# Performance work log

Measured on AMD Instinct MI355X. Metric: run time of the kernel, lower is better.

Reference implementation:

```python
import jax, jax.numpy as jnp
import numpy as np

EPS = 1e-5
POW = 0.5

def _eig_fun(X, fn):
    # symmetric matrix function via eigendecomposition: V f(diag) V^T
    w, V = jnp.linalg.eigh(X)
    return jnp.einsum('...ij,...j,...kj->...ik', V, fn(w), V)

def sym_pow(X, p):
    return _eig_fun(X, lambda w: jnp.power(w, p))

def sym_log(X):
    return _eig_fun(X, jnp.log)

def sym_exp(X):
    return _eig_fun(X, jnp.exp)

def exp_at(T, G):
    # Riemannian exp of tangent T at base point G (affine-invariant metric)
    Gh = sym_pow(G, 0.5)
    Gnh = sym_pow(G, -0.5)
    return Gh @ sym_exp(Gnh @ T @ Gnh) @ Gh

def bary_geom(X, n_iter=1):
    # Karcher/geodesic mean of batch of SPD matrices X: (B, n, n)
    # init at arithmetic mean, n_iter Karcher flow steps
    G = jnp.mean(X, axis=0)
    for _ in range(n_iter):
        Gh = sym_pow(G, 0.5)
        Gnh = sym_pow(G, -0.5)
        T = jnp.mean(sym_log(Gnh @ X @ Gnh), axis=0)
        G = Gh @ sym_exp(T) @ Gh
    return G

def setup_inputs() -> dict:
    key = jax.random.key(0)
    N, h, n = 256, 16, 64
    k1, k2, k3 = jax.random.split(key, 3)
    A = jax.random.normal(k1, (N, h, n, n), dtype=jnp.float32)
    # well-conditioned SPD inputs with distinct eigenvalues
    X = A @ jnp.swapaxes(A, -1, -2) / n + 0.5 * jnp.eye(n, dtype=jnp.float32)
    Bw = jax.random.normal(k2, (n, n), dtype=jnp.float32) * 0.1
    weight = sym_exp(0.5 * (Bw + Bw.T))  # SPD parameter near identity
    Bm = jax.random.normal(k3, (n, n), dtype=jnp.float32) * 0.1
    M = sym_exp(0.5 * (Bm + Bm.T))       # SPD deformation parameter
    shift = jnp.ones((1,), dtype=jnp.float32)
    return {"X": X, "weight": weight, "M": M, "shift": shift}

def reference(X, weight, M, shift):
    N, h, n, _ = X.shape
    Xb = X.reshape(N * h, n, n)
    Xp = sym_pow(Xb, POW)                  # PowerEig(X, po)
    Mnh = sym_pow(M, -0.5)
    Mh = sym_pow(M, 0.5)
    Xc = Mnh @ Xp @ Mnh                    # CongrG(., M, 'neg')
    Wp = sym_pow(weight, POW)              # PowerEig(weight, po)
    Wc = Mnh @ Wp @ Mnh                    # CongrG1(weight, M, 'neg')

    mean = bary_geom(Xc)                   # BaryGeom (training path)
    mnh = sym_pow(mean, -0.5)
    # pal1(mean, LogG(Xc, mean)) = PT of Riemannian log to identity
    T = sym_log(mnh @ Xc @ mnh)            # (N*h, n, n) tangent at I
    # cal_var: mean squared Riemannian distance to the mean
    var = jnp.mean(jnp.sum(T * T, axis=(-2, -1)))
    T = T * (shift[0] / jnp.sqrt(var + EPS))  # scale1
    Wh = sym_pow(weight, 0.5)
    S = Wh @ T @ Wh                        # pal2(weight, LogG1(.))
    Y = exp_at(S, Wc)                      # ExpG(., weight_deformed)
    Y = Mh @ Y @ Mh                        # CongrG(., M, 'pos')
    Y = sym_pow(Y, 1.0 / POW)              # PowerEig(., 1/po)
    return Y.reshape(N, h, n, n)
```

## Files before the change

### kernel.cpp

```cpp
#include <hip/hip_runtime.h>
#include <math.h>

#define PITCH 72
#define NP 68
#define SW_BATCH 12
#define SW_SMALL 10
#define NPART 32
#define EPS2_ROT 1e-12f

#define KATTR __attribute__((amdgpu_flat_work_group_size(256, 256), amdgpu_waves_per_eu(1, 2)))

#define OFF_ACCG 0
#define OFF_ACCT (NPART*4096)
#define OFF_BASE (2*NPART*4096)
#define SL_MNH  (OFF_BASE + 0*4096)
#define SL_MH   (OFF_BASE + 1*4096)
#define SL_WH   (OFF_BASE + 2*4096)
#define SL_P    (OFF_BASE + 3*4096)
#define SL_Q    (OFF_BASE + 4*4096)
#define SL_GH   (OFF_BASE + 5*4096)
#define SL_GNH  (OFF_BASE + 6*4096)
#define SL_MNH2 (OFF_BASE + 7*4096)
#define SL_WCH  (OFF_BASE + 8*4096)
#define OFF_VAR (OFF_BASE + 9*4096)
#define SL_SC   (OFF_BASE + 9*4096 + 1)

struct __align__(16) F4 { float v[4]; };

struct __align__(16) Smem {
  float S0[64*PITCH];
  float S1[64*PITCH];
  float w2[64];
  float wc[64];
  float red[256];
};

__device__ __forceinline__ void g2s(float* dst, const float* __restrict__ src) {
  int t = threadIdx.x;
#pragma unroll
  for (int i = 0; i < 4; ++i) {
    int e4 = t + (i << 8);
    F4 vv = *(const F4*)&src[e4 * 4];
    *(F4*)&dst[(e4 >> 4) * PITCH + (e4 & 15) * 4] = vv;
  }
  __syncthreads();
}
__device__ __forceinline__ void s2g(float* __restrict__ dst, const float* src) {
  int t = threadIdx.x;
#pragma unroll
  for (int i = 0; i < 4; ++i) {
    int e4 = t + (i << 8);
    F4 vv = *(const F4*)&src[(e4 >> 4) * PITCH + (e4 & 15) * 4];
    *(F4*)&dst[e4 * 4] = vv;
  }
  __syncthreads();
}

template<int MODE>
__device__ void mmX(Smem& sm) {
  int t = threadIdx.x;
  int R0 = t >> 4;
  int J = (t & 15) * 4;
  float acc[4][4] = {};
  for (int kb = 0; kb < 64; kb += 4) {
    F4 a4[4], b4[4];
#pragma unroll
    for (int i = 0; i < 4; ++i) {
      const float* L = (MODE == 0) ? sm.S1 : sm.S0;
      a4[i] = *(const F4*)&L[(R0 + 16 * i) * PITCH + kb];
    }
#pragma unroll
    for (int kk = 0; kk < 4; ++kk) {
      const float* Rp = (MODE == 0) ? sm.S0 : sm.S1;
      b4[kk] = *(const F4*)&Rp[(kb + kk) * PITCH + J];
    }
#pragma unroll
    for (int i = 0; i < 4; ++i)
#pragma unroll
      for (int kk = 0; kk < 4; ++kk)
#pragma unroll
        for (int m = 0; m < 4; ++m)
          acc[i][m] = fmaf(a4[i].v[kk], b4[kk].v[m], acc[i][m]);
  }
  __syncthreads();
#pragma unroll
  for (int i = 0; i < 4; ++i) {
    F4 o;
#pragma unroll
    for (int m = 0; m < 4; ++m) o.v[m] = acc[i][m];
    *(F4*)&sm.S0[(R0 + 16 * i) * PITCH + J] = o;
  }
  __syncthreads();
}

__device__ void reconT(Smem& sm) {
  __syncthreads();
  int t = threadIdx.x;
  int R0 = t >> 4;
  int J = (t & 15) * 4;
  float acc[4][4] = {};
  for (int k = 0; k < 64; ++k) {
    float w = sm.wc[k];
    float a[4];
#pragma unroll
    for (int i = 0; i < 4; ++i) a[i] = w * sm.S0[k * PITCH + R0 + 16 * i];
    F4 b = *(const F4*)&sm.S0[k * PITCH + J];
#pragma unroll
    for (int i = 0; i < 4; ++i)
#pragma unroll
      for (int m = 0; m < 4; ++m) acc[i][m] = fmaf(a[i], b.v[m], acc[i][m]);
  }
#pragma unroll
  for (int i = 0; i < 4; ++i) {
    F4 o;
#pragma unroll
    for (int m = 0; m < 4; ++m) o.v[m] = acc[i][m];
    *(F4*)&sm.S1[(R0 + 16 * i) * PITCH + J] = o;
  }
  __syncthreads();
}

__device__ float frob2(Smem& sm) {
  int t = threadIdx.x;
  float s = 0.f;
#pragma unroll
  for (int i = 0; i < 4; ++i) {
    int e4 = t + (i << 8);
    F4 vv = *(const F4*)&sm.S0[(e4 >> 4) * PITCH + (e4 & 15) * 4];
#pragma unroll
    for (int m = 0; m < 4; ++m) s = fmaf(vv.v[m], vv.v[m], s);
  }
  sm.red[t] = s;
  __syncthreads();
  for (int o = 128; o; o >>= 1) { if (t < o) sm.red[t] += sm.red[t + o]; __syncthreads(); }
  float f = sm.red[0];
  __syncthreads();
  return f;
}

__device__ __forceinline__ void hestenes_reg(float (&own)[64], float& w2out, int sweeps) {
  const int lane = threadIdx.x & 63;
  float nrm = 0.f;
#pragma unroll
  for (int i = 0; i < 64; ++i) nrm = fmaf(own[i], own[i], nrm);

  for (int s = 0; s < sweeps; ++s) {
    bool any = false;
    for (int m = 1; m < 64; ++m) {
      const int paddr = ((lane ^ m) << 2);
      float pv[64];
#pragma unroll
      for (int i = 0; i < 64; ++i)
        asm volatile("ds_bpermute_b32 %0, %1, %2"
                     : "=v"(pv[i]) : "v"(paddr), "v"(own[i]));
      asm volatile("s_waitcnt lgkmcnt(0)" ::: "memory");
      __builtin_amdgcn_sched_barrier(0);
      float d0 = 0.f, d1 = 0.f, d2 = 0.f, d3 = 0.f;
#pragma unroll
      for (int i = 0; i < 64; i += 4) {
        d0 = fmaf(own[i + 0], pv[i + 0], d0);
        d1 = fmaf(own[i + 1], pv[i + 1], d1);
        d2 = fmaf(own[i + 2], pv[i + 2], d2);
        d3 = fmaf(own[i + 3], pv[i + 3], d3);
      }
      float d = (d0 + d1) + (d2 + d3);
      float pn = __shfl_xor(nrm, m);
      if (d * d > EPS2_ROT * (nrm * pn)) {
        any = true;
        bool lo = lane < (lane ^ m);
        float dpp = lo ? nrm : pn;
        float dqq = lo ? pn : nrm;
        float tau = (dqq - dpp) * (0.5f * __builtin_amdgcn_rcpf(d));
        float tt = __builtin_amdgcn_rcpf(fabsf(tau) +
                                         __builtin_amdgcn_sqrtf(fmaf(tau, tau, 1.f)));
        if (tau < 0.f) tt = -tt;
        float c = __builtin_amdgcn_rsqf(fmaf(tt, tt, 1.f));
        float s_ = tt * c;
        float sg = lo ? -s_ : s_;
#pragma unroll
        for (int i = 0; i < 64; ++i) own[i] = fmaf(sg, pv[i], c * own[i]);
        float td = tt * d;
        nrm += lo ? -td : td;
      }
    }
    if (!__any((int)any)) break;
  }
  float w = 0.f;
#pragma unroll
  for (int i = 0; i < 64; ++i) w = fmaf(own[i], own[i], w);
  w2out = w;
}

__device__ void hestenes_small(Smem& sm, int sweeps) {
  const int t = threadIdx.x;
  if (t < 64) {
    float own[64];
#pragma unroll
    for (int i = 0; i < 64; ++i) own[i] = sm.S0[t * PITCH + i];
    float w2;
    hestenes_reg(own, w2, sweeps);
#pragma unroll
    for (int i = 0; i < 64; ++i) sm.S0[t * PITCH + i] = own[i];
    sm.w2[t] = w2;
  }
  __syncthreads();
}

struct __align__(16) SmemK {
  float A[64*NP];
  float Bop[64*NP];
  float wc[64];
  float red[256];
};
struct __align__(16) SmemK4 {
  float A[64*NP];
  float P[64*NP];
  float Q[64*NP];
  float wc[64];
  float red[256];
};

__device__ __forceinline__ void g2s68(float* dst, const float* __restrict__ src) {
  int t = threadIdx.x;
#pragma unroll
  for (int i = 0; i < 4; ++i) {
    int e4 = t + (i << 8);
    F4 vv = *(const F4*)&src[e4 * 4];
    *(F4*)&dst[(e4 >> 4) * NP + (e4 & 15) * 4] = vv;
  }
  __syncthreads();
}
__device__ __forceinline__ void g2s68s(float* dst, const float* __restrict__ src, float sc) {
  int t = threadIdx.x;
#pragma unroll
  for (int i = 0; i < 4; ++i) {
    int e4 = t + (i << 8);
    F4 vv = *(const F4*)&src[e4 * 4];
#pragma unroll
    for (int m = 0; m < 4; ++m) vv.v[m] *= sc;
    *(F4*)&dst[(e4 >> 4) * NP + (e4 & 15) * 4] = vv;
  }
  __syncthreads();
}

template<int MODE>
__device__ void mm68(float* A, const float* Bo) {
  int t = threadIdx.x;
  int R0 = t >> 4;
  if (MODE == 2) {
    int J0 = t & 15;
    float acc[4][4] = {};
    for (int kb = 0; kb < 64; kb += 4) {
      F4 a4[4];
#pragma unroll
      for (int i = 0; i < 4; ++i) a4[i] = *(const F4*)&A[(R0 + 16 * i) * NP + kb];
#pragma unroll
      for (int kk = 0; kk < 4; ++kk) {
        float b[4];
#pragma unroll
        for (int m = 0; m < 4; ++m) b[m] = Bo[(J0 + 16 * m) * NP + kb + kk];
#pragma unroll
        for (int i = 0; i < 4; ++i)
#pragma unroll
          for (int m = 0; m < 4; ++m) acc[i][m] = fmaf(a4[i].v[kk], b[m], acc[i][m]);
      }
    }
    __syncthreads();
#pragma unroll
    for (int i = 0; i < 4; ++i)
#pragma unroll
      for (int m = 0; m < 4; ++m)
        A[(R0 + 16 * i) * NP + J0 + 16 * m] = acc[i][m];
    __syncthreads();
  } else {
    int J = (t & 15) * 4;
    float acc[4][4] = {};
    for (int kb = 0; kb < 64; kb += 4) {
      F4 a4[4], b4[4];
#pragma unroll
      for (int i = 0; i < 4; ++i) {
        const float* L = (MODE == 0) ? Bo : A;
        a4[i] = *(const F4*)&L[(R0 + 16 * i) * NP + kb];
      }
#pragma unroll
      for (int kk = 0; kk < 4; ++kk) {
        const float* Rp = (MODE == 0) ? A : Bo;
        b4[kk] = *(const F4*)&Rp[(kb + kk) * NP + J];
      }
#pragma unroll
      for (int i = 0; i < 4; ++i)
#pragma unroll
        for (int kk = 0; kk < 4; ++kk)
#pragma unroll
          for (int m = 0; m < 4; ++m)
            acc[i][m] = fmaf(a4[i].v[kk], b4[kk].v[m], acc[i][m]);
    }
    __syncthreads();
#pragma unroll
    for (int i = 0; i < 4; ++i) {
      F4 o;
#pragma unroll
      for (int m = 0; m < 4; ++m) o.v[m] = acc[i][m];
      *(F4*)&A[(R0 + 16 * i) * NP + J] = o;
    }
    __syncthreads();
  }
}

__device__ float frob68(const float* A, float* red) {
  int t = threadIdx.x;
  float s = 0.f;
#pragma unroll
  for (int i = 0; i < 4; ++i) {
    int e4 = t + (i << 8);
    F4 vv = *(const F4*)&A[(e4 >> 4) * NP + (e4 & 15) * 4];
#pragma unroll
    for (int m = 0; m < 4; ++m) s = fmaf(vv.v[m], vv.v[m], s);
  }
  red[t] = s;
  __syncthreads();
  for (int o = 128; o; o >>= 1) { if (t < o) red[t] += red[t + o]; __syncthreads(); }
  float f = red[0];
  __syncthreads();
  return f;
}

__device__ void msq_store(const float* Z, float* __restrict__ gout) {
  int t = threadIdx.x;
  int R0 = t >> 4;
  int J = (t & 15) * 4;
  float acc[4][4] = {};
  for (int kb = 0; kb < 64; kb += 4) {
    F4 a4[4], b4[4];
#pragma unroll
    for (int i = 0; i < 4; ++i) a4[i] = *(const F4*)&Z[(R0 + 16 * i) * NP + kb];
#pragma unroll
    for (int kk = 0; kk < 4; ++kk) b4[kk] = *(const F4*)&Z[(kb + kk) * NP + J];
#pragma unroll
    for (int i = 0; i < 4; ++i)
#pragma unroll
      for (int kk = 0; kk < 4; ++kk)
#pragma unroll
        for (int m = 0; m < 4; ++m)
          acc[i][m] = fmaf(a4[i].v[kk], b4[kk].v[m], acc[i][m]);
  }
#pragma unroll
  for (int i = 0; i < 4; ++i) {
    F4 o;
#pragma unroll
    for (int m = 0; m < 4; ++m) o.v[m] = acc[i][m];
    *(F4*)&gout[(R0 + 16 * i) * 64 + J] = o;
  }
}


__global__ __launch_bounds__(256) void kzero(float* ws) {
  int i = blockIdx.x * 256 + threadIdx.x;
  if (i < OFF_BASE) ws[i] = 0.f;
  if (i == 0) ws[OFF_VAR] = 0.f;
}

__global__ KATTR void kprep(const float* __restrict__ weight,
                            const float* __restrict__ M,
                            float* ws) {
  __shared__ Smem sm;
  int t = threadIdx.x;
  g2s(sm.S0, M);
  hestenes_small(sm, SW_SMALL);
  if (t < 64) sm.wc[t] = powf(fmaxf(sm.w2[t], 1e-12f), -1.25f);
  reconT(sm); s2g(ws + SL_MNH, sm.S1);
  if (t < 64) sm.wc[t] = powf(fmaxf(sm.w2[t], 1e-12f), -0.75f);
  reconT(sm); s2g(ws + SL_MH, sm.S1);

  g2s(sm.S0, weight);
  hestenes_small(sm, SW_SMALL);
  if (t < 64) sm.wc[t] = powf(fmaxf(sm.w2[t], 1e-12f), -0.75f);
  reconT(sm); s2g(ws + SL_WH, sm.S1);

  g2s(sm.S0, ws + SL_MNH);
  mmX<1>(sm);
  g2s(sm.S1, ws + SL_MNH);
  mmX<1>(sm);
  hestenes_small(sm, SW_SMALL);
  if (t < 64) sm.wc[t] = powf(fmaxf(sm.w2[t], 1e-12f), -0.75f);
  reconT(sm); s2g(ws + SL_WCH, sm.S1);
  if (t < 64) sm.wc[t] = powf(fmaxf(sm.w2[t], 1e-12f), -1.25f);
  reconT(sm);
  g2s(sm.S0, ws + SL_WH);
  mmX<0>(sm);
  s2g(ws + SL_P, sm.S0);
  g2s(sm.S0, ws + SL_WCH);
  g2s(sm.S1, ws + SL_MH);
  mmX<0>(sm);
  s2g(ws + SL_Q, sm.S0);
}

__global__ KATTR void k1(const float* __restrict__ X,
                         float* __restrict__ out, float* ws) {
  __shared__ SmemK sm;
  int t = threadIdx.x;
  int w = t >> 6, lane = t & 63;
  size_t b = blockIdx.x;
  g2s68(sm.Bop, ws + SL_MNH);

  float own[64]; float w2;
  {
    const float* Xm = X + (b * 4 + w) * 4096 + (size_t)lane * 64;
#pragma unroll
    for (int j = 0; j < 16; ++j) {
      F4 r = *(const F4*)&Xm[4 * j];
      own[4 * j + 0] = r.v[0]; own[4 * j + 1] = r.v[1];
      own[4 * j + 2] = r.v[2]; own[4 * j + 3] = r.v[3];
    }
  }
  hestenes_reg(own, w2, SW_BATCH);
  __syncthreads();

  int R0 = t >> 4, J = (t & 15) * 4;
  for (int m = 0; m < 4; ++m) {
    if (w == m) {
#pragma unroll
      for (int j = 0; j < 16; ++j) {
        F4 o = {{own[4 * j], own[4 * j + 1], own[4 * j + 2], own[4 * j + 3]}};
        *(F4*)&sm.A[lane * NP + 4 * j] = o;
      }
      sm.wc[lane] = powf(fmaxf(w2, 1e-12f), -0.75f);
    }
    __syncthreads();
    mm68<1>(sm.A, sm.Bop);
    float acc[4][4] = {};
    for (int k = 0; k < 64; ++k) {
      float wck = sm.wc[k];
      float a[4];
#pragma unroll
      for (int i = 0; i < 4; ++i) a[i] = wck * sm.A[k * NP + R0 + 16 * i];
      F4 bb = *(const F4*)&sm.A[k * NP + J];
#pragma unroll
      for (int i = 0; i < 4; ++i)
#pragma unroll
        for (int mc = 0; mc < 4; ++mc) acc[i][mc] = fmaf(a[i], bb.v[mc], acc[i][mc]);
    }
    float* Xc = out + (b * 4 + m) * 4096;
    float* accp = ws + OFF_ACCG + (size_t)((b * 4 + m) & (NPART - 1)) * 4096;
#pragma unroll
    for (int i = 0; i < 4; ++i) {
      F4 o;
#pragma unroll
      for (int mc = 0; mc < 4; ++mc) o.v[mc] = acc[i][mc];
      int base = (R0 + 16 * i) * 64 + J;
      *(F4*)&Xc[base] = o;
#pragma unroll
      for (int mc = 0; mc < 4; ++mc) atomicAdd(accp + base + mc, o.v[mc]);
    }
    __syncthreads();
  }
}

__global__ KATTR void ksmall2(float* ws, float invB) {
  __shared__ Smem sm;
  int t = threadIdx.x;
#pragma unroll
  for (int i = 0; i < 4; ++i) {
    int e4 = t + (i << 8);
    F4 sum = {{0.f, 0.f, 0.f, 0.f}};
    for (int p = 0; p < NPART; ++p) {
      F4 vv = *(const F4*)&ws[OFF_ACCG + p * 4096 + e4 * 4];
#pragma unroll
      for (int m = 0; m < 4; ++m) sum.v[m] += vv.v[m];
    }
#pragma unroll
    for (int m = 0; m < 4; ++m) sum.v[m] *= invB;
    *(F4*)&sm.S0[(e4 >> 4) * PITCH + (e4 & 15) * 4] = sum;
  }
  __syncthreads();
  hestenes_small(sm, SW_SMALL);
  if (t < 64) sm.wc[t] = powf(fmaxf(sm.w2[t], 1e-12f), -0.75f);
  reconT(sm); s2g(ws + SL_GH, sm.S1);
  if (t < 64) sm.wc[t] = powf(fmaxf(sm.w2[t], 1e-12f), -1.25f);
  reconT(sm); s2g(ws + SL_GNH, sm.S1);
}

__global__ KATTR void k2(const float* __restrict__ XcBuf, float* ws) {
  __shared__ SmemK sm;
  int t = threadIdx.x;
  int w = t >> 6, lane = t & 63;
  size_t b = blockIdx.x;
  g2s68(sm.Bop, ws + SL_GNH);

  float own[64]; float w2;
  for (int m = 0; m < 4; ++m) {
    g2s68(sm.A, XcBuf + (b * 4 + m) * 4096);
    mm68<1>(sm.A, sm.Bop);
    mm68<0>(sm.A, sm.Bop);
    if (w == m) {
#pragma unroll
      for (int i = 0; i < 64; ++i) own[i] = sm.A[i * NP + lane];
    }
    __syncthreads();
  }
  hestenes_reg(own, w2, SW_BATCH);
  __syncthreads();

  int R0 = t >> 4, J = (t & 15) * 4;
  for (int m = 0; m < 4; ++m) {
    if (w == m) {
#pragma unroll
      for (int j = 0; j < 16; ++j) {
        F4 o = {{own[4 * j], own[4 * j + 1], own[4 * j + 2], own[4 * j + 3]}};
        *(F4*)&sm.A[lane * NP + 4 * j] = o;
      }
      float s2 = fmaxf(w2, 1e-12f);
      sm.wc[lane] = 0.5f * logf(s2) / s2;
    }
    __syncthreads();
    float acc[4][4] = {};
    for (int k = 0; k < 64; ++k) {
      float wck = sm.wc[k];
      float a[4];
#pragma unroll
      for (int i = 0; i < 4; ++i) a[i] = wck * sm.A[k * NP + R0 + 16 * i];
      F4 bb = *(const F4*)&sm.A[k * NP + J];
#pragma unroll
      for (int i = 0; i < 4; ++i)
#pragma unroll
        for (int mc = 0; mc < 4; ++mc) acc[i][mc] = fmaf(a[i], bb.v[mc], acc[i][mc]);
    }
    float* accp = ws + OFF_ACCT + (size_t)((b * 4 + m) & (NPART - 1)) * 4096;
#pragma unroll
    for (int i = 0; i < 4; ++i) {
      int base = (R0 + 16 * i) * 64 + J;
#pragma unroll
      for (int mc = 0; mc < 4; ++mc) atomicAdd(accp + base + mc, acc[i][mc]);
    }
    __syncthreads();
  }
}

__global__ KATTR void ksmall3(float* ws, float invB) {
  __shared__ Smem sm;
  int t = threadIdx.x;
#pragma unroll
  for (int i = 0; i < 4; ++i) {
    int e4 = t + (i << 8);
    F4 sum = {{0.f, 0.f, 0.f, 0.f}};
    for (int p = 0; p < NPART; ++p) {
      F4 vv = *(const F4*)&ws[OFF_ACCT + p * 4096 + e4 * 4];
#pragma unroll
      for (int m = 0; m < 4; ++m) sum.v[m] += vv.v[m];
    }
#pragma unroll
    for (int m = 0; m < 4; ++m) sum.v[m] *= invB;
    *(F4*)&sm.S0[(e4 >> 4) * PITCH + (e4 & 15) * 4] = sum;
  }
  __syncthreads();
  float mu = sqrtf(frob2(sm)) + 1e-3f;
  if (t < 64) sm.S0[t * PITCH + t] += mu;
  __syncthreads();
  hestenes_small(sm, SW_SMALL);
  if (t < 64) {
    float s2 = fmaxf(sm.w2[t], 1e-12f);
    sm.wc[t] = expf(sqrtf(s2) - mu) / s2;
  }
  reconT(sm);
  g2s(sm.S0, ws + SL_GH);
  mmX<1>(sm);
  g2s(sm.S1, ws + SL_GH);
  mmX<1>(sm);
  hestenes_small(sm, SW_SMALL);
  if (t < 64) sm.wc[t] = powf(fmaxf(sm.w2[t], 1e-12f), -1.25f);
  reconT(sm); s2g(ws + SL_MNH2, sm.S1);
}

__global__ KATTR void k3(float* __restrict__ buf, float* ws) {
  __shared__ SmemK sm;
  int t = threadIdx.x;
  int w = t >> 6, lane = t & 63;
  size_t b = blockIdx.x;
  g2s68(sm.Bop, ws + SL_MNH2);

  float own[64]; float w2;
  for (int m = 0; m < 4; ++m) {
    g2s68(sm.A, buf + (b * 4 + m) * 4096);
    mm68<1>(sm.A, sm.Bop);
    mm68<0>(sm.A, sm.Bop);
    if (w == m) {
#pragma unroll
      for (int i = 0; i < 64; ++i) own[i] = sm.A[i * NP + lane];
    }
    __syncthreads();
  }
  hestenes_reg(own, w2, SW_BATCH);
  __syncthreads();

  int R0 = t >> 4, J = (t & 15) * 4;
  for (int m = 0; m < 4; ++m) {
    if (w == m) {
#pragma unroll
      for (int j = 0; j < 16; ++j) {
        F4 o = {{own[4 * j], own[4 * j + 1], own[4 * j + 2], own[4 * j + 3]}};
        *(F4*)&sm.A[lane * NP + 4 * j] = o;
      }
      float s2 = fmaxf(w2, 1e-12f);
      sm.wc[lane] = 0.5f * logf(s2) / s2;
    }
    __syncthreads();
    float acc[4][4] = {};
    for (int k = 0; k < 64; ++k) {
      float wck = sm.wc[k];
      float a[4];
#pragma unroll
      for (int i = 0; i < 4; ++i) a[i] = wck * sm.A[k * NP + R0 + 16 * i];
      F4 bb = *(const F4*)&sm.A[k * NP + J];
#pragma unroll
      for (int i = 0; i < 4; ++i)
#pragma unroll
        for (int mc = 0; mc < 4; ++mc) acc[i][mc] = fmaf(a[i], bb.v[mc], acc[i][mc]);
    }
    float* Tg = buf + (b * 4 + m) * 4096;
    float ssq = 0.f;
#pragma unroll
    for (int i = 0; i < 4; ++i) {
      F4 o;
#pragma unroll
      for (int mc = 0; mc < 4; ++mc) o.v[mc] = acc[i][mc];
      int base = (R0 + 16 * i) * 64 + J;
      *(F4*)&Tg[base] = o;
#pragma unroll
      for (int mc = 0; mc < 4; ++mc) ssq = fmaf(o.v[mc], o.v[mc], ssq);
    }
    sm.red[t] = ssq;
    __syncthreads();
    for (int o = 128; o; o >>= 1) { if (t < o) sm.red[t] += sm.red[t + o]; __syncthreads(); }
    if (t == 0) atomicAdd(ws + OFF_VAR, sm.red[0]);
    __syncthreads();
  }
}

__global__ void kscale(float* ws, const float* __restrict__ shift, float invB) {
  if (threadIdx.x == 0 && blockIdx.x == 0) {
    float var = ws[OFF_VAR] * invB;
    ws[SL_SC] = shift[0] / sqrtf(var + 1e-5f);
  }
}

__global__ KATTR void k4(float* __restrict__ buf, float* ws) {
  __shared__ SmemK4 sm;
  int t = threadIdx.x;
  int w = t >> 6, lane = t & 63;
  size_t b = blockIdx.x;
  float sc = ws[SL_SC];
  g2s68(sm.P, ws + SL_P);
  g2s68(sm.Q, ws + SL_Q);

  float own[64]; float w2; float muw = 0.f;
  for (int m = 0; m < 4; ++m) {
    g2s68s(sm.A, buf + (b * 4 + m) * 4096, sc);
    mm68<0>(sm.A, sm.P);
    mm68<2>(sm.A, sm.P);
    float f = frob68(sm.A, sm.red);
    if (w == m) {
      muw = sqrtf(f) + 1e-3f;
#pragma unroll
      for (int i = 0; i < 64; ++i) {
        float v = sm.A[i * NP + lane];
        own[i] = v + ((i == lane) ? muw : 0.f);
      }
    }
    __syncthreads();
  }
  hestenes_reg(own, w2, SW_BATCH);
  __syncthreads();

  int R0 = t >> 4, J = (t & 15) * 4;
  for (int m = 0; m < 4; ++m) {
    if (w == m) {
#pragma unroll
      for (int j = 0; j < 16; ++j) {
        F4 o = {{own[4 * j], own[4 * j + 1], own[4 * j + 2], own[4 * j + 3]}};
        *(F4*)&sm.A[lane * NP + 4 * j] = o;
      }
      float s2 = fmaxf(w2, 1e-12f);
      sm.wc[lane] = expf(sqrtf(s2) - muw) / s2;
    }
    __syncthreads();
    mm68<2>(sm.A, sm.Q);
    float acc[4][4] = {};
    for (int k = 0; k < 64; ++k) {
      float wck = sm.wc[k];
      float a[4];
#pragma unroll
      for (int i = 0; i < 4; ++i) a[i] = wck * sm.A[k * NP + R0 + 16 * i];
      F4 bb = *(const F4*)&sm.A[k * NP + J];
#pragma unroll
      for (int i = 0; i < 4; ++i)
#pragma unroll
        for (int mc = 0; mc < 4; ++mc) acc[i][mc] = fmaf(a[i], bb.v[mc], acc[i][mc]);
    }
#pragma unroll
    for (int i = 0; i < 4; ++i) {
      F4 o;
#pragma unroll
      for (int mc = 0; mc < 4; ++mc) o.v[mc] = acc[i][mc];
      *(F4*)&sm.P[(R0 + 16 * i) * NP + J] = o;
    }
    __syncthreads();
    msq_store(sm.P, buf + (b * 4 + m) * 4096);
    __syncthreads();
  }
}

extern "C" void kernel_launch(void* const* d_in, const int* in_sizes, int n_in,
                              void* d_out, int out_size, void* d_ws, size_t ws_size,
                              hipStream_t stream) {
  const float* X      = (const float*)d_in[0];
  const float* weight = (const float*)d_in[1];
  const float* M      = (const float*)d_in[2];
  const float* shift  = (const float*)d_in[3];
  float* out = (float*)d_out;
  float* ws  = (float*)d_ws;
  int B = in_sizes[0] / 4096;
  float invB = 1.f / (float)B;
  int G = B / 4;

  hipLaunchKernelGGL(kzero,   dim3(OFF_BASE / 256), dim3(256), 0, stream, ws);
  hipLaunchKernelGGL(kprep,   dim3(1), dim3(256), 0, stream, weight, M, ws);
  hipLaunchKernelGGL(k1,      dim3(G), dim3(256), 0, stream, X, out, ws);
  hipLaunchKernelGGL(ksmall2, dim3(1), dim3(256), 0, stream, ws, invB);
  hipLaunchKernelGGL(k2,      dim3(G), dim3(256), 0, stream, out, ws);
  hipLaunchKernelGGL(ksmall3, dim3(1), dim3(256), 0, stream, ws, invB);
  hipLaunchKernelGGL(k3,      dim3(G), dim3(256), 0, stream, out, ws);
  hipLaunchKernelGGL(kscale,  dim3(1), dim3(64), 0, stream, ws, shift, invB);
  hipLaunchKernelGGL(k4,      dim3(G), dim3(256), 0, stream, out, ws);
}
```

Before: 9.408 ms.

## Split Jacobi eigensolver into standalone 64-thread kernel, separate GEMM stages

Moves the one-sided Hestenes Jacobi sweep out of the fused 256-thread kernels into a dedicated 64-thread-per-matrix kernel launched once per stage. Each GEMM/congruence stage becomes its own high-occupancy kernel that reads the rotated columns back and recomputes the squared eigenvalues from row norms. k3 now uses a precomputed combined matrix R and a pre-kernel instead of re-running congruence inside the eigensolver kernel. It also swaps inline-asm bpermute for __shfl_xor. The goal is to decouple the register-heavy eigensolver from the LDS-heavy matmuls so each can reach better occupancy, at the cost of extra launches and extra global round-trips of the batch buffer.

```diff
diff --git a/kernel.cpp b/kernel.cpp
--- a/kernel.cpp
+++ b/kernel.cpp
@@ -8,14 +8,13 @@
 #define NPART 32
 #define EPS2_ROT 1e-12f
 
-#define KATTR __attribute__((amdgpu_flat_work_group_size(256, 256), amdgpu_waves_per_eu(1, 2)))
-
 #define OFF_ACCG 0
 #define OFF_ACCT (NPART*4096)
 #define OFF_BASE (2*NPART*4096)
 #define SL_MNH  (OFF_BASE + 0*4096)
 #define SL_MH   (OFF_BASE + 1*4096)
 #define SL_WH   (OFF_BASE + 2*4096)
+#define SL_MU   SL_WH
 #define SL_P    (OFF_BASE + 3*4096)
 #define SL_Q    (OFF_BASE + 4*4096)
 #define SL_GH   (OFF_BASE + 5*4096)
@@ -24,119 +23,9 @@
 #define SL_WCH  (OFF_BASE + 8*4096)
 #define OFF_VAR (OFF_BASE + 9*4096)
 #define SL_SC   (OFF_BASE + 9*4096 + 1)
+#define SL_R    (OFF_BASE + 10*4096)
 
 struct __align__(16) F4 { float v[4]; };
-
-struct __align__(16) Smem {
-  float S0[64*PITCH];
-  float S1[64*PITCH];
-  float w2[64];
-  float wc[64];
-  float red[256];
-};
-
-__device__ __forceinline__ void g2s(float* dst, const float* __restrict__ src) {
-  int t = threadIdx.x;
-#pragma unroll
-  for (int i = 0; i < 4; ++i) {
-    int e4 = t + (i << 8);
-    F4 vv = *(const F4*)&src[e4 * 4];
-    *(F4*)&dst[(e4 >> 4) * PITCH + (e4 & 15) * 4] = vv;
-  }
-  __syncthreads();
-}
-__device__ __forceinline__ void s2g(float* __restrict__ dst, const float* src) {
-  int t = threadIdx.x;
-#pragma unroll
-  for (int i = 0; i < 4; ++i) {
-    int e4 = t + (i << 8);
-    F4 vv = *(const F4*)&src[(e4 >> 4) * PITCH + (e4 & 15) * 4];
-    *(F4*)&dst[e4 * 4] = vv;
-  }
-  __syncthreads();
-}
-
-template<int MODE>
-__device__ void mmX(Smem& sm) {
-  int t = threadIdx.x;
-  int R0 = t >> 4;
-  int J = (t & 15) * 4;
-  float acc[4][4] = {};
-  for (int kb = 0; kb < 64; kb += 4) {
-    F4 a4[4], b4[4];
-#pragma unroll
-    for (int i = 0; i < 4; ++i) {
-      const float* L = (MODE == 0) ? sm.S1 : sm.S0;
-      a4[i] = *(const F4*)&L[(R0 + 16 * i) * PITCH + kb];
-    }
-#pragma unroll
-    for (int kk = 0; kk < 4; ++kk) {
-      const float* Rp = (MODE == 0) ? sm.S0 : sm.S1;
-      b4[kk] = *(const F4*)&Rp[(kb + kk) * PITCH + J];
-    }
-#pragma unroll
-    for (int i = 0; i < 4; ++i)
-#pragma unroll
-      for (int kk = 0; kk < 4; ++kk)
-#pragma unroll
-        for (int m = 0; m < 4; ++m)
-          acc[i][m] = fmaf(a4[i].v[kk], b4[kk].v[m], acc[i][m]);
-  }
-  __syncthreads();
-#pragma unroll
-  for (int i = 0; i < 4; ++i) {
-    F4 o;
-#pragma unroll
-    for (int m = 0; m < 4; ++m) o.v[m] = acc[i][m];
-    *(F4*)&sm.S0[(R0 + 16 * i) * PITCH + J] = o;
-  }
-  __syncthreads();
-}
-
-__device__ void reconT(Smem& sm) {
-  __syncthreads();
-  int t = threadIdx.x;
-  int R0 = t >> 4;
-  int J = (t & 15) * 4;
-  float acc[4][4] = {};
-  for (int k = 0; k < 64; ++k) {
-    float w = sm.wc[k];
-    float a[4];
-#pragma unroll
-    for (int i = 0; i < 4; ++i) a[i] = w * sm.S0[k * PITCH + R0 + 16 * i];
-    F4 b = *(const F4*)&sm.S0[k * PITCH + J];
-#pragma unroll
-    for (int i = 0; i < 4; ++i)
-#pragma unroll
-      for (int m = 0; m < 4; ++m) acc[i][m] = fmaf(a[i], b.v[m], acc[i][m]);
-  }
-#pragma unroll
-  for (int i = 0; i < 4; ++i) {
-    F4 o;
-#pragma unroll
-    for (int m = 0; m < 4; ++m) o.v[m] = acc[i][m];
-    *(F4*)&sm.S1[(R0 + 16 * i) * PITCH + J] = o;
-  }
-  __syncthreads();
-}
-
-__device__ float frob2(Smem& sm) {
-  int t = threadIdx.x;
-  float s = 0.f;
-#pragma unroll
-  for (int i = 0; i < 4; ++i) {
-    int e4 = t + (i << 8);
-    F4 vv = *(const F4*)&sm.S0[(e4 >> 4) * PITCH + (e4 & 15) * 4];
-#pragma unroll
-    for (int m = 0; m < 4; ++m) s = fmaf(vv.v[m], vv.v[m], s);
-  }
-  sm.red[t] = s;
-  __syncthreads();
-  for (int o = 128; o; o >>= 1) { if (t < o) sm.red[t] += sm.red[t + o]; __syncthreads(); }
-  float f = sm.red[0];
-  __syncthreads();
-  return f;
-}
 
 __device__ __forceinline__ void hestenes_reg(float (&own)[64], float& w2out, int sweeps) {
   const int lane = threadIdx.x & 63;
@@ -147,14 +36,9 @@
   for (int s = 0; s < sweeps; ++s) {
     bool any = false;
     for (int m = 1; m < 64; ++m) {
-      const int paddr = ((lane ^ m) << 2);
       float pv[64];
 #pragma unroll
-      for (int i = 0; i < 64; ++i)
-        asm volatile("ds_bpermute_b32 %0, %1, %2"
-                     : "=v"(pv[i]) : "v"(paddr), "v"(own[i]));
-      asm volatile("s_waitcnt lgkmcnt(0)" ::: "memory");
-      __builtin_amdgcn_sched_barrier(0);
+      for (int i = 0; i < 64; ++i) pv[i] = __shfl_xor(own[i], m);
       float d0 = 0.f, d1 = 0.f, d2 = 0.f, d3 = 0.f;
 #pragma unroll
       for (int i = 0; i < 64; i += 4) {
@@ -191,6 +75,139 @@
   w2out = w;
 }
 
+__global__ __launch_bounds__(64, 1) void keig(float* __restrict__ buf,
+                                              const float* __restrict__ src) {
+  const int l = threadIdx.x;
+  const size_t b = blockIdx.x;
+  const float* Sm = src + b * 4096 + (size_t)l * 64;
+  float own[64];
+#pragma unroll
+  for (int j = 0; j < 16; ++j) {
+    F4 r = *(const F4*)&Sm[4 * j];
+    own[4 * j + 0] = r.v[0]; own[4 * j + 1] = r.v[1];
+    own[4 * j + 2] = r.v[2]; own[4 * j + 3] = r.v[3];
+  }
+  float w2;
+  hestenes_reg(own, w2, SW_BATCH);
+  float* Dm = buf + b * 4096 + (size_t)l * 64;
+#pragma unroll
+  for (int j = 0; j < 16; ++j) {
+    F4 o = {{own[4 * j], own[4 * j + 1], own[4 * j + 2], own[4 * j + 3]}};
+    *(F4*)&Dm[4 * j] = o;
+  }
+}
+
+struct __align__(16) Smem {
+  float S0[64*PITCH];
+  float S1[64*PITCH];
+  float w2[64];
+  float wc[64];
+  float red[256];
+};
+
+__device__ __forceinline__ void g2s(float* dst, const float* __restrict__ src) {
+  int t = threadIdx.x;
+#pragma unroll
+  for (int i = 0; i < 4; ++i) {
+    int e4 = t + (i << 8);
+    F4 vv = *(const F4*)&src[e4 * 4];
+    *(F4*)&dst[(e4 >> 4) * PITCH + (e4 & 15) * 4] = vv;
+  }
+  __syncthreads();
+}
+__device__ __forceinline__ void s2g(float* __restrict__ dst, const float* src) {
+  int t = threadIdx.x;
+#pragma unroll
+  for (int i = 0; i < 4; ++i) {
+    int e4 = t + (i << 8);
+    F4 vv = *(const F4*)&src[(e4 >> 4) * PITCH + (e4 & 15) * 4];
+    *(F4*)&dst[e4 * 4] = vv;
+  }
+  __syncthreads();
+}
+
+template<int MODE>
+__device__ void mmX(Smem& sm) {
+  int t = threadIdx.x;
+  int R0 = t >> 4;
+  int J = (t & 15) * 4;
+  float acc[4][4] = {};
+  for (int kb = 0; kb < 64; kb += 4) {
+    F4 a4[4], b4[4];
+#pragma unroll
+    for (int i = 0; i < 4; ++i) {
+      const float* L = (MODE == 0) ? sm.S1 : sm.S0;
+      a4[i] = *(const F4*)&L[(R0 + 16 * i) * PITCH + kb];
+    }
+#pragma unroll
+    for (int kk = 0; kk < 4; ++kk) {
+      const float* Rp = (MODE == 0) ? sm.S0 : sm.S1;
+      b4[kk] = *(const F4*)&Rp[(kb + kk) * PITCH + J];
+    }
+#pragma unroll
+    for (int i = 0; i < 4; ++i)
+#pragma unroll
+      for (int kk = 0; kk < 4; ++kk)
+#pragma unroll
+        for (int m = 0; m < 4; ++m)
+          acc[i][m] = fmaf(a4[i].v[kk], b4[kk].v[m], acc[i][m]);
+  }
+  __syncthreads();
+#pragma unroll
+  for (int i = 0; i < 4; ++i) {
+    F4 o;
+#pragma unroll
+    for (int m = 0; m < 4; ++m) o.v[m] = acc[i][m];
+    *(F4*)&sm.S0[(R0 + 16 * i) * PITCH + J] = o;
+  }
+  __syncthreads();
+}
+
+__device__ void reconT(Smem& sm) {
+  __syncthreads();
+  int t = threadIdx.x;
+  int R0 = t >> 4;
+  int J = (t & 15) * 4;
+  float acc[4][4] = {};
+  for (int k = 0; k < 64; ++k) {
+    float w = sm.wc[k];
+    float a[4];
+#pragma unroll
+    for (int i = 0; i < 4; ++i) a[i] = w * sm.S0[k * PITCH + R0 + 16 * i];
+    F4 b = *(const F4*)&sm.S0[k * PITCH + J];
+#pragma unroll
+    for (int i = 0; i < 4; ++i)
+#pragma unroll
+      for (int m = 0; m < 4; ++m) acc[i][m] = fmaf(a[i], b.v[m], acc[i][m]);
+  }
+#pragma unroll
+  for (int i = 0; i < 4; ++i) {
+    F4 o;
+#pragma unroll
+    for (int m = 0; m < 4; ++m) o.v[m] = acc[i][m];
+    *(F4*)&sm.S1[(R0 + 16 * i) * PITCH + J] = o;
+  }
+  __syncthreads();
+}
+
+__device__ float frob2(Smem& sm) {
+  int t = threadIdx.x;
+  float s = 0.f;
+#pragma unroll
+  for (int i = 0; i < 4; ++i) {
+    int e4 = t + (i << 8);
+    F4 vv = *(const F4*)&sm.S0[(e4 >> 4) * PITCH + (e4 & 15) * 4];
+#pragma unroll
+    for (int m = 0; m < 4; ++m) s = fmaf(vv.v[m], vv.v[m], s);
+  }
+  sm.red[t] = s;
+  __syncthreads();
+  for (int o = 128; o; o >>= 1) { if (t < o) sm.red[t] += sm.red[t + o]; __syncthreads(); }
+  float f = sm.red[0];
+  __syncthreads();
+  return f;
+}
+
 __device__ void hestenes_small(Smem& sm, int sweeps) {
   const int t = threadIdx.x;
   if (t < 64) {
@@ -212,13 +229,6 @@
   float wc[64];
   float red[256];
 };
-struct __align__(16) SmemK4 {
-  float A[64*NP];
-  float P[64*NP];
-  float Q[64*NP];
-  float wc[64];
-  float red[256];
-};
 
 __device__ __forceinline__ void g2s68(float* dst, const float* __restrict__ src) {
   int t = threadIdx.x;
@@ -241,6 +251,23 @@
     *(F4*)&dst[(e4 >> 4) * NP + (e4 & 15) * 4] = vv;
   }
   __syncthreads();
+}
+__device__ __forceinline__ void s2g68(float* __restrict__ dst, const float* src) {
+  int t = threadIdx.x;
+#pragma unroll
+  for (int i = 0; i < 4; ++i) {
+    int e4 = t + (i << 8);
+    F4 vv = *(const F4*)&src[(e4 >> 4) * NP + (e4 & 15) * 4];
+    *(F4*)&dst[e4 * 4] = vv;
+  }
+  __syncthreads();
+}
+
+__device__ __forceinline__ float rown2(const float* A, int t) {
+  float s = 0.f;
+#pragma unroll
+  for (int j = 0; j < 64; ++j) { float v = A[t * NP + j]; s = fmaf(v, v, s); }
+  return fmaxf(s, 1e-12f);
 }
 
 template<int MODE>
@@ -360,9 +387,9 @@
   if (i == 0) ws[OFF_VAR] = 0.f;
 }
 
-__global__ KATTR void kprep(const float* __restrict__ weight,
-                            const float* __restrict__ M,
-                            float* ws) {
+__global__ __launch_bounds__(256, 1) void kprep(const float* __restrict__ weight,
+                                                const float* __restrict__ M,
+                                                float* ws) {
   __shared__ Smem sm;
   int t = threadIdx.x;
   g2s(sm.S0, M);
@@ -395,37 +422,16 @@
   s2g(ws + SL_Q, sm.S0);
 }
 
-__global__ KATTR void k1(const float* __restrict__ X,
-                         float* __restrict__ out, float* ws) {
+__global__ __launch_bounds__(256, 4) void k1b(float* __restrict__ buf, float* ws) {
   __shared__ SmemK sm;
   int t = threadIdx.x;
-  int w = t >> 6, lane = t & 63;
   size_t b = blockIdx.x;
   g2s68(sm.Bop, ws + SL_MNH);
-
-  float own[64]; float w2;
-  {
-    const float* Xm = X + (b * 4 + w) * 4096 + (size_t)lane * 64;
-#pragma unroll
-    for (int j = 0; j < 16; ++j) {
-      F4 r = *(const F4*)&Xm[4 * j];
-      own[4 * j + 0] = r.v[0]; own[4 * j + 1] = r.v[1];
-      own[4 * j + 2] = r.v[2]; own[4 * j + 3] = r.v[3];
-    }
-  }
-  hestenes_reg(own, w2, SW_BATCH);
-  __syncthreads();
-
   int R0 = t >> 4, J = (t & 15) * 4;
   for (int m = 0; m < 4; ++m) {
-    if (w == m) {
-#pragma unroll
-      for (int j = 0; j < 16; ++j) {
-        F4 o = {{own[4 * j], own[4 * j + 1], own[4 * j + 2], own[4 * j + 3]}};
-        *(F4*)&sm.A[lane * NP + 4 * j] = o;
-      }
-      sm.wc[lane] = powf(fmaxf(w2, 1e-12f), -0.75f);
-    }
+    size_t bm = b * 4 + m;
+    g2s68(sm.A, buf + bm * 4096);
+    if (t < 64) sm.wc[t] = powf(rown2(sm.A, t), -0.75f);
     __syncthreads();
     mm68<1>(sm.A, sm.Bop);
     float acc[4][4] = {};
@@ -440,8 +446,8 @@
 #pragma unroll
         for (int mc = 0; mc < 4; ++mc) acc[i][mc] = fmaf(a[i], bb.v[mc], acc[i][mc]);
     }
-    float* Xc = out + (b * 4 + m) * 4096;
-    float* accp = ws + OFF_ACCG + (size_t)((b * 4 + m) & (NPART - 1)) * 4096;
+    float* Xc = buf + bm * 4096;
+    float* accp = ws + OFF_ACCG + (size_t)(bm & (NPART - 1)) * 4096;
 #pragma unroll
     for (int i = 0; i < 4; ++i) {
       F4 o;
@@ -456,7 +462,7 @@
   }
 }
 
-__global__ KATTR void ksmall2(float* ws, float invB) {
+__global__ __launch_bounds__(256, 1) void ksmall2(float* ws, float invB) {
   __shared__ Smem sm;
   int t = threadIdx.x;
 #pragma unroll
@@ -480,37 +486,30 @@
   reconT(sm); s2g(ws + SL_GNH, sm.S1);
 }
 
-__global__ KATTR void k2(const float* __restrict__ XcBuf, float* ws) {
+__global__ __launch_bounds__(256, 4) void kcongr(float* __restrict__ buf, float* ws) {
   __shared__ SmemK sm;
-  int t = threadIdx.x;
-  int w = t >> 6, lane = t & 63;
   size_t b = blockIdx.x;
   g2s68(sm.Bop, ws + SL_GNH);
-
-  float own[64]; float w2;
   for (int m = 0; m < 4; ++m) {
-    g2s68(sm.A, XcBuf + (b * 4 + m) * 4096);
+    size_t bm = b * 4 + m;
+    g2s68(sm.A, buf + bm * 4096);
     mm68<1>(sm.A, sm.Bop);
     mm68<0>(sm.A, sm.Bop);
-    if (w == m) {
-#pragma unroll
-      for (int i = 0; i < 64; ++i) own[i] = sm.A[i * NP + lane];
-    }
-    __syncthreads();
-  }
-  hestenes_reg(own, w2, SW_BATCH);
-  __syncthreads();
-
+    s2g68(buf + bm * 4096, sm.A);
+  }
+}
+
+__global__ __launch_bounds__(256, 4) void k2b(const float* __restrict__ buf, float* ws) {
+  __shared__ SmemK sm;
+  int t = threadIdx.x;
+  size_t b = blockIdx.x;
   int R0 = t >> 4, J = (t & 15) * 4;
   for (int m = 0; m < 4; ++m) {
-    if (w == m) {
-#pragma unroll
-      for (int j = 0; j < 16; ++j) {
-        F4 o = {{own[4 * j], own[4 * j + 1], own[4 * j + 2], own[4 * j + 3]}};
-        *(F4*)&sm.A[lane * NP + 4 * j] = o;
-      }
-      float s2 = fmaxf(w2, 1e-12f);
-      sm.wc[lane] = 0.5f * logf(s2) / s2;
+    size_t bm = b * 4 + m;
+    g2s68(sm.A, buf + bm * 4096);
+    if (t < 64) {
+      float s2 = rown2(sm.A, t);
+      sm.wc[t] = 0.5f * logf(s2) / s2;
     }
     __syncthreads();
     float acc[4][4] = {};
@@ -525,7 +524,7 @@
 #pragma unroll
         for (int mc = 0; mc < 4; ++mc) acc[i][mc] = fmaf(a[i], bb.v[mc], acc[i][mc]);
     }
-    float* accp = ws + OFF_ACCT + (size_t)((b * 4 + m) & (NPART - 1)) * 4096;
+    float* accp = ws + OFF_ACCT + (size_t)(bm & (NPART - 1)) * 4096;
 #pragma unroll
     for (int i = 0; i < 4; ++i) {
       int base = (R0 + 16 * i) * 64 + J;
@@ -536,7 +535,7 @@
   }
 }
 
-__global__ KATTR void ksmall3(float* ws, float invB) {
+__global__ __launch_bounds__(256, 1) void ksmall3(float* ws, float invB) {
   __shared__ Smem sm;
   int t = threadIdx.x;
 #pragma unroll
@@ -569,41 +568,24 @@
   hestenes_small(sm, SW_SMALL);
   if (t < 64) sm.wc[t] = powf(fmaxf(sm.w2[t], 1e-12f), -1.25f);
   reconT(sm); s2g(ws + SL_MNH2, sm.S1);
-}
-
-__global__ KATTR void k3(float* __restrict__ buf, float* ws) {
+  g2s(sm.S0, ws + SL_MNH2);
+  g2s(sm.S1, ws + SL_GH);
+  mmX<1>(sm);
+  s2g(ws + SL_R, sm.S0);
+}
+
+__global__ __launch_bounds__(256, 4) void k3pre(float* __restrict__ buf, float* ws) {
   __shared__ SmemK sm;
   int t = threadIdx.x;
-  int w = t >> 6, lane = t & 63;
   size_t b = blockIdx.x;
-  g2s68(sm.Bop, ws + SL_MNH2);
-
-  float own[64]; float w2;
-  for (int m = 0; m < 4; ++m) {
-    g2s68(sm.A, buf + (b * 4 + m) * 4096);
-    mm68<1>(sm.A, sm.Bop);
-    mm68<0>(sm.A, sm.Bop);
-    if (w == m) {
-#pragma unroll
-      for (int i = 0; i < 64; ++i) own[i] = sm.A[i * NP + lane];
-    }
-    __syncthreads();
-  }
-  hestenes_reg(own, w2, SW_BATCH);
-  __syncthreads();
-
+  g2s68(sm.Bop, ws + SL_R);
   int R0 = t >> 4, J = (t & 15) * 4;
   for (int m = 0; m < 4; ++m) {
-    if (w == m) {
-#pragma unroll
-      for (int j = 0; j < 16; ++j) {
-        F4 o = {{own[4 * j], own[4 * j + 1], own[4 * j + 2], own[4 * j + 3]}};
-        *(F4*)&sm.A[lane * NP + 4 * j] = o;
-      }
-      float s2 = fmaxf(w2, 1e-12f);
-      sm.wc[lane] = 0.5f * logf(s2) / s2;
-    }
-    __syncthreads();
+    size_t bm = b * 4 + m;
+    g2s68(sm.A, buf + bm * 4096);
+    if (t < 64) sm.wc[t] = powf(rown2(sm.A, t), -0.5f);
+    __syncthreads();
+    mm68<2>(sm.A, sm.Bop);
     float acc[4][4] = {};
     for (int k = 0; k < 64; ++k) {
       float wck = sm.wc[k];
@@ -616,7 +598,44 @@
 #pragma unroll
         for (int mc = 0; mc < 4; ++mc) acc[i][mc] = fmaf(a[i], bb.v[mc], acc[i][mc]);
     }
-    float* Tg = buf + (b * 4 + m) * 4096;
+    float* Bg = buf + bm * 4096;
+#pragma unroll
+    for (int i = 0; i < 4; ++i) {
+      F4 o;
+#pragma unroll
+      for (int mc = 0; mc < 4; ++mc) o.v[mc] = acc[i][mc];
+      *(F4*)&Bg[(R0 + 16 * i) * 64 + J] = o;
+    }
+    __syncthreads();
+  }
+}
+
+__global__ __launch_bounds__(256, 4) void k3b(float* __restrict__ buf, float* ws) {
+  __shared__ SmemK sm;
+  int t = threadIdx.x;
+  size_t b = blockIdx.x;
+  int R0 = t >> 4, J = (t & 15) * 4;
+  for (int m = 0; m < 4; ++m) {
+    size_t bm = b * 4 + m;
+    g2s68(sm.A, buf + bm * 4096);
+    if (t < 64) {
+      float s2 = rown2(sm.A, t);
+      sm.wc[t] = 0.5f * logf(s2) / s2;
+    }
+    __syncthreads();
+    float acc[4][4] = {};
+    for (int k = 0; k < 64; ++k) {
+      float wck = sm.wc[k];
+      float a[4];
+#pragma unroll
+      for (int i = 0; i < 4; ++i) a[i] = wck * sm.A[k * NP + R0 + 16 * i];
+      F4 bb = *(const F4*)&sm.A[k * NP + J];
+#pragma unroll
+      for (int i = 0; i < 4; ++i)
+#pragma unroll
+        for (int mc = 0; mc < 4; ++mc) acc[i][mc] = fmaf(a[i], bb.v[mc], acc[i][mc]);
+    }
+    float* Tg = buf + bm * 4096;
     float ssq = 0.f;
 #pragma unroll
     for (int i = 0; i < 4; ++i) {
@@ -643,47 +662,51 @@
   }
 }
 
-__global__ KATTR void k4(float* __restrict__ buf, float* ws) {
-  __shared__ SmemK4 sm;
-  int t = threadIdx.x;
-  int w = t >> 6, lane = t & 63;
+__global__ __launch_bounds__(256, 4) void k4pre(float* __restrict__ buf, float* ws) {
+  __shared__ SmemK sm;
+  int t = threadIdx.x;
   size_t b = blockIdx.x;
   float sc = ws[SL_SC];
-  g2s68(sm.P, ws + SL_P);
-  g2s68(sm.Q, ws + SL_Q);
-
-  float own[64]; float w2; float muw = 0.f;
+  g2s68(sm.Bop, ws + SL_P);
   for (int m = 0; m < 4; ++m) {
-    g2s68s(sm.A, buf + (b * 4 + m) * 4096, sc);
-    mm68<0>(sm.A, sm.P);
-    mm68<2>(sm.A, sm.P);
+    size_t bm = b * 4 + m;
+    g2s68s(sm.A, buf + bm * 4096, sc);
+    mm68<0>(sm.A, sm.Bop);
+    mm68<2>(sm.A, sm.Bop);
     float f = frob68(sm.A, sm.red);
-    if (w == m) {
-      muw = sqrtf(f) + 1e-3f;
-#pragma unroll
-      for (int i = 0; i < 64; ++i) {
-        float v = sm.A[i * NP + lane];
-        own[i] = v + ((i == lane) ? muw : 0.f);
-      }
-    }
-    __syncthreads();
-  }
-  hestenes_reg(own, w2, SW_BATCH);
-  __syncthreads();
-
+    float mu = sqrtf(f) + 1e-3f;
+    if (t == 0) ws[SL_MU + bm] = mu;
+    float* Sg = buf + bm * 4096;
+#pragma unroll
+    for (int i = 0; i < 4; ++i) {
+      int e4 = t + (i << 8);
+      int row = e4 >> 4;
+      F4 v = *(const F4*)&sm.A[row * NP + (e4 & 15) * 4];
+#pragma unroll
+      for (int mc = 0; mc < 4; ++mc)
+        if ((e4 & 15) * 4 + mc == row) v.v[mc] += mu;
+      *(F4*)&Sg[e4 * 4] = v;
+    }
+    __syncthreads();
+  }
+}
+
+__global__ __launch_bounds__(256, 4) void k4b(float* __restrict__ buf, float* ws) {
+  __shared__ SmemK sm;
+  int t = threadIdx.x;
+  size_t b = blockIdx.x;
   int R0 = t >> 4, J = (t & 15) * 4;
   for (int m = 0; m < 4; ++m) {
-    if (w == m) {
-#pragma unroll
-      for (int j = 0; j < 16; ++j) {
-        F4 o = {{own[4 * j], own[4 * j + 1], own[4 * j + 2], own[4 * j + 3]}};
-        *(F4*)&sm.A[lane * NP + 4 * j] = o;
-      }
-      float s2 = fmaxf(w2, 1e-12f);
-      sm.wc[lane] = expf(sqrtf(s2) - muw) / s2;
-    }
-    __syncthreads();
-    mm68<2>(sm.A, sm.Q);
+    size_t bm = b * 4 + m;
+    g2s68(sm.A, buf + bm * 4096);
+    float mu = ws[SL_MU + bm];
+    if (t < 64) {
+      float s2 = rown2(sm.A, t);
+      sm.wc[t] = expf(sqrtf(s2) - mu) / s2;
+    }
+    __syncthreads();
+    g2s68(sm.Bop, ws + SL_Q);
+    mm68<2>(sm.A, sm.Bop);
     float acc[4][4] = {};
     for (int k = 0; k < 64; ++k) {
       float wck = sm.wc[k];
@@ -701,10 +724,10 @@
       F4 o;
 #pragma unroll
       for (int mc = 0; mc < 4; ++mc) o.v[mc] = acc[i][mc];
-      *(F4*)&sm.P[(R0 + 16 * i) * NP + J] = o;
-    }
-    __syncthreads();
-    msq_store(sm.P, buf + (b * 4 + m) * 4096);
+      *(F4*)&sm.Bop[(R0 + 16 * i) * NP + J] = o;
+    }
+    __syncthreads();
+    msq_store(sm.Bop, buf + bm * 4096);
     __syncthreads();
   }
 }
@@ -724,11 +747,18 @@
 
   hipLaunchKernelGGL(kzero,   dim3(OFF_BASE / 256), dim3(256), 0, stream, ws);
   hipLaunchKernelGGL(kprep,   dim3(1), dim3(256), 0, stream, weight, M, ws);
-  hipLaunchKernelGGL(k1,      dim3(G), dim3(256), 0, stream, X, out, ws);
+  hipLaunchKernelGGL(keig,    dim3(B), dim3(64), 0, stream, out, X);
+  hipLaunchKernelGGL(k1b,     dim3(G), dim3(256), 0, stream, out, ws);
   hipLaunchKernelGGL(ksmall2, dim3(1), dim3(256), 0, stream, ws, invB);
-  hipLaunchKernelGGL(k2,      dim3(G), dim3(256), 0, stream, out, ws);
+  hipLaunchKernelGGL(kcongr,  dim3(G), dim3(256), 0, stream, out, ws);
+  hipLaunchKernelGGL(keig,    dim3(B), dim3(64), 0, stream, out, out);
+  hipLaunchKernelGGL(k2b,     dim3(G), dim3(256), 0, stream, out, ws);
   hipLaunchKernelGGL(ksmall3, dim3(1), dim3(256), 0, stream, ws, invB);
-  hipLaunchKernelGGL(k3,      dim3(G), dim3(256), 0, stream, out, ws);
+  hipLaunchKernelGGL(k3pre,   dim3(G), dim3(256), 0, stream, out, ws);
+  hipLaunchKernelGGL(keig,    dim3(B), dim3(64), 0, stream, out, out);
+  hipLaunchKernelGGL(k3b,     dim3(G), dim3(256), 0, stream, out, ws);
   hipLaunchKernelGGL(kscale,  dim3(1), dim3(64), 0, stream, ws, shift, invB);
-  hipLaunchKernelGGL(k4,      dim3(G), dim3(256), 0, stream, out, ws);
-}
+  hipLaunchKernelGGL(k4pre,   dim3(G), dim3(256), 0, stream, out, ws);
+  hipLaunchKernelGGL(keig,    dim3(B), dim3(64), 0, stream, out, out);
+  hipLaunchKernelGGL(k4b,     dim3(G), dim3(256), 0, stream, out, ws);
+}
```

New measurement: 11.09 ms. +17.9%, slower.
